# Optimization experiments

Hardware: AMD Instinct MI355X
Metric: run time of the kernel (lower is better)

## Reference

```python
import jax, jax.numpy as jnp
import numpy as np

RNN = 512
ENC = 512
HID = 512
ATT_SIZE = 196
B = 1024


def setup_inputs() -> dict:
    key = jax.random.key(0)
    ks = jax.random.split(key, 20)
    s = 0.02
    d = {
        "h": jax.random.normal(ks[0], (B, RNN), jnp.float32),
        "sentinel": jax.random.normal(ks[1], (B, RNN), jnp.float32),
        "att_feats": jax.random.normal(ks[2], (B, ATT_SIZE, RNN), jnp.float32),
        "W_ctx2att": jax.random.normal(ks[3], (RNN, HID), jnp.float32) * s,
        "b_ctx2att": jnp.zeros((HID,), jnp.float32),
        "W_sl": jax.random.normal(ks[4], (RNN, ENC), jnp.float32) * s,
        "b_sl": jnp.zeros((ENC,), jnp.float32),
        "W_se": jax.random.normal(ks[5], (ENC, HID), jnp.float32) * s,
        "b_se": jnp.zeros((HID,), jnp.float32),
        "W_hl": jax.random.normal(ks[6], (RNN, ENC), jnp.float32) * s,
        "b_hl": jnp.zeros((ENC,), jnp.float32),
        "W_he": jax.random.normal(ks[7], (ENC, HID), jnp.float32) * s,
        "b_he": jnp.zeros((HID,), jnp.float32),
        "W_alpha": jax.random.normal(ks[8], (HID, 1), jnp.float32) * s,
        "b_alpha": jnp.zeros((1,), jnp.float32),
        "W_att2h": jax.random.normal(ks[9], (RNN, RNN), jnp.float32) * s,
        "b_att2h": jnp.zeros((RNN,), jnp.float32),
    }
    return d


def reference(h, sentinel, att_feats, W_ctx2att, b_ctx2att, W_sl, b_sl,
              W_se, b_se, W_hl, b_hl, W_he, b_he, W_alpha, b_alpha,
              W_att2h, b_att2h):
    # Eval mode: dropout is identity.
    # Project attention features: [B, 196, HID]
    p_att = jnp.einsum("bsd,dh->bsh", att_feats, W_ctx2att) + b_ctx2att
    # Sentinel branch
    sent_lin = jax.nn.relu(sentinel @ W_sl + b_sl)          # [B, ENC]
    sent_emb = sent_lin @ W_se + b_se                       # [B, HID]
    # Hidden-state branch
    h_lin = jnp.tanh(h @ W_hl + b_hl)                       # [B, ENC]
    h_emb = h_lin @ W_he + b_he                             # [B, HID]
    # Concat sentinel with visual features: [B, 197, *]
    img_all = jnp.concatenate([sent_lin[:, None, :], att_feats], axis=1)
    img_all_embed = jnp.concatenate([sent_emb[:, None, :], p_att], axis=1)
    # Additive attention scores over 197 positions
    hA = jnp.tanh(img_all_embed + h_emb[:, None, :])        # [B, 197, HID]
    scores = (jnp.einsum("bsh,ho->bso", hA, W_alpha) + b_alpha)[..., 0]  # [B, 197]
    alpha = jax.nn.softmax(scores, axis=-1)
    # Weighted context
    cHat = jnp.einsum("bs,bsd->bd", alpha, img_all)          # [B, RNN]
    atten_out = cHat + h_lin
    out = jnp.tanh(atten_out @ W_att2h + b_att2h)            # [B, RNN]
    return out
```

## Files before the change

kernel.cpp:

```cpp
#include <hip/hip_runtime.h>
#include <hip/hip_bf16.h>

#define KDIM 512
#define NDIM 512
#define ATT  196
#define NB   1024

typedef __attribute__((ext_vector_type(8))) short bf16x8;
typedef __attribute__((ext_vector_type(8))) unsigned short ushort8;
typedef __attribute__((ext_vector_type(4))) float f32x4;

typedef const __attribute__((address_space(1))) unsigned int gas_uint;
typedef __attribute__((address_space(3))) unsigned int las_uint;

__device__ __forceinline__ void gload16(const void* g, void* l) {
    __builtin_amdgcn_global_load_lds((gas_uint*)g, (las_uint*)l, 16, 0, 0);
}

__device__ __forceinline__ float fast_tanh(float x) {
    x = fminf(15.f, fmaxf(-15.f, x));
    float t = __expf(2.f * x);
    return (t - 1.f) / (t + 1.f);
}

__device__ __forceinline__ unsigned short f2bf(float x) {
    union { float f; unsigned u; } v; v.f = x;
    unsigned r = v.u + 0x7FFF + ((v.u >> 16) & 1);
    return (unsigned short)(r >> 16);
}

__device__ __forceinline__ unsigned pk2(float a, float b) {
    __hip_bfloat162 h = __float22bfloat162_rn(float2{a, b});
    union { __hip_bfloat162 h2; unsigned u; } c; c.h2 = h;
    return c.u;
}

__global__ __launch_bounds__(256) void prep_weights(
        const float* __restrict__ W0, const float* __restrict__ W1,
        const float* __restrict__ W2, const float* __restrict__ W3,
        const float* __restrict__ W4, const float* __restrict__ W5,
        unsigned short* __restrict__ Wt) {
    int w = blockIdx.x >> 6;
    int t = blockIdx.x & 63;
    int k0 = (t >> 3) << 6, n0 = (t & 7) << 6;
    const float* W = (w == 0) ? W0 : (w == 1) ? W1 : (w == 2) ? W2 :
                     (w == 3) ? W3 : (w == 4) ? W4 : W5;
    __shared__ float tile[64][65];
    int tid = threadIdx.x;
    int nc = tid & 15, kr = tid >> 4;
#pragma unroll
    for (int i = 0; i < 4; ++i) {
        int k = kr + i * 16;
        float4 v = *(const float4*)&W[(size_t)(k0 + k) * NDIM + n0 + nc * 4];
        tile[k][nc * 4 + 0] = v.x; tile[k][nc * 4 + 1] = v.y;
        tile[k][nc * 4 + 2] = v.z; tile[k][nc * 4 + 3] = v.w;
    }
    __syncthreads();
    int n = tid >> 2, ks = tid & 3;
    ushort8 v0, v1;
#pragma unroll
    for (int j = 0; j < 8; ++j) v0[j] = f2bf(tile[ks * 16 + j][n]);
#pragma unroll
    for (int j = 0; j < 8; ++j) v1[j] = f2bf(tile[ks * 16 + 8 + j][n]);
    size_t base = ((size_t)w << 18) + (size_t)(n0 + n) * KDIM + k0 + ks * 16;
    *(ushort8*)&Wt[base] = v0;
    *(ushort8*)&Wt[base + 8] = v1;
}

__global__ __launch_bounds__(256) void gemm64(
        const float* __restrict__ A0, const unsigned short* __restrict__ W0,
        const float* __restrict__ bia0, float* __restrict__ O0, int act0,
        const float* __restrict__ A1, const unsigned short* __restrict__ W1,
        const float* __restrict__ bia1, float* __restrict__ O1, int act1) {
    const int op = blockIdx.y;
    const float* A = op ? A1 : A0;
    const unsigned short* Bt = op ? W1 : W0;
    const float* bias = op ? bia1 : bia0;
    float* out = op ? O1 : O0;
    const int act = op ? act1 : act0;

    __shared__ unsigned short A_lds[2][64 * 32];
    __shared__ unsigned short B_lds[2][128 * 32];

    const int tid = threadIdx.x;
    const int gm0 = (blockIdx.x >> 2) * 64, gn0 = (blockIdx.x & 3) * 128;
    const int wid = tid >> 6, lane = tid & 63;
    const int wm = wid >> 1, wn = wid & 1;
    const int lr = lane & 15, lk = lane >> 4;

    const int arow = tid >> 2, akc = tid & 3;
    const float* aptr = A + (size_t)(gm0 + arow) * KDIM + akc * 8;
    const int aoff = arow * 32 + ((akc ^ ((arow >> 1) & 3)) << 3);

    auto stageB = [&](int kt, int buf) {
#pragma unroll
        for (int j = 0; j < 2; ++j) {
            int c = tid + j * 256;
            int col = c >> 2, slot = c & 3;
            const unsigned short* src = Bt + (size_t)(gn0 + col) * KDIM +
                                        ((slot ^ ((col >> 1) & 3)) << 3) + kt * 32;
            gload16(src, &B_lds[buf][c * 8]);
        }
    };

    f32x4 acc[2][4] = {};

    {
        float4 x0 = *(const float4*)aptr;
        float4 x1 = *(const float4*)(aptr + 4);
        stageB(0, 0);
        uint4 p;
        p.x = pk2(x0.x, x0.y); p.y = pk2(x0.z, x0.w);
        p.z = pk2(x1.x, x1.y); p.w = pk2(x1.z, x1.w);
        *(uint4*)&A_lds[0][aoff] = p;
    }
    __syncthreads();

    const int swk = ((lk ^ ((lr >> 1) & 3)) << 3);
    for (int kt = 0; kt < 16; ++kt) {
        const int buf = kt & 1;
        float4 x0, x1;
        if (kt < 15) {
            const float* ap = aptr + (kt + 1) * 32;
            x0 = *(const float4*)ap;
            x1 = *(const float4*)(ap + 4);
            stageB(kt + 1, buf ^ 1);
        }
        bf16x8 af[2], bfr[4];
#pragma unroll
        for (int m = 0; m < 2; ++m)
            af[m] = *(const bf16x8*)&A_lds[buf][(wm * 32 + m * 16 + lr) * 32 + swk];
#pragma unroll
        for (int n = 0; n < 4; ++n)
            bfr[n] = *(const bf16x8*)&B_lds[buf][(wn * 64 + n * 16 + lr) * 32 + swk];
#pragma unroll
        for (int m = 0; m < 2; ++m)
#pragma unroll
            for (int n = 0; n < 4; ++n)
                acc[m][n] = __builtin_amdgcn_mfma_f32_16x16x32_bf16(af[m], bfr[n], acc[m][n], 0, 0, 0);
        if (kt < 15) {
            uint4 p;
            p.x = pk2(x0.x, x0.y); p.y = pk2(x0.z, x0.w);
            p.z = pk2(x1.x, x1.y); p.w = pk2(x1.z, x1.w);
            *(uint4*)&A_lds[buf ^ 1][aoff] = p;
        }
        __syncthreads();
    }

#pragma unroll
    for (int m = 0; m < 2; ++m)
#pragma unroll
        for (int n = 0; n < 4; ++n) {
            int col = gn0 + wn * 64 + n * 16 + lr;
            float bsv = bias[col];
#pragma unroll
            for (int r = 0; r < 4; ++r) {
                int row = gm0 + wm * 32 + m * 16 + lk * 4 + r;
                float v = acc[m][n][r] + bsv;
                if (act == 0) v = fmaxf(v, 0.f);
                else if (act == 1) v = fast_tanh(v);
                out[(size_t)row * NDIM + col] = v;
            }
        }
}

__launch_bounds__(256, 3)
__global__ void gemm_score(const float* __restrict__ A,
                           const unsigned short* __restrict__ Bt,
                           const float* __restrict__ b_ctx,
                           const float* __restrict__ h_emb,
                           const float* __restrict__ Walpha,
                           float* __restrict__ score) {
    __shared__ unsigned short A_lds[2][128 * 32];
    __shared__ unsigned short B_lds[2][128 * 32];
    __shared__ float ch_s[2][128];
    __shared__ float wa_s[128];
    __shared__ float s_red[2][128];

    const int tid  = threadIdx.x;
    const int bidx = blockIdx.x;
    const int xcd  = bidx & 7, u = bidx >> 3;
    const int mblk = xcd * 196 + (u >> 2), nblk = u & 3;
    const int gm0  = mblk * 128, gn0 = nblk * 128;

    const int wid = tid >> 6, lane = tid & 63;
    const int wm  = wid >> 1, wn = wid & 1;
    const int lr  = lane & 15, lk = lane >> 4;

    const int b0 = gm0 / ATT;
    {
        int j = tid >> 7, cloc = tid & 127;
        int bb = b0 + j; if (bb > NB - 1) bb = NB - 1;
        ch_s[j][cloc] = b_ctx[gn0 + cloc] + h_emb[(size_t)bb * NDIM + gn0 + cloc];
        if (tid < 128) wa_s[tid] = Walpha[gn0 + tid];
    }

    const int arow = tid >> 1, ahalf = tid & 1;
    const float* aptr = A + (size_t)(gm0 + arow) * KDIM + ahalf * 16;
    const int skc0  = (ahalf * 2) ^ ((arow >> 1) & 3);
    const int aoff0 = arow * 32 + skc0 * 8;
    const int aoff1 = arow * 32 + (skc0 ^ 1) * 8;

    auto stageB = [&](int kt, int buf) {
#pragma unroll
        for (int j = 0; j < 2; ++j) {
            int c = tid + j * 256;
            int col = c >> 2, slot = c & 3;
            const unsigned short* src = Bt + (size_t)(gn0 + col) * KDIM +
                                        ((slot ^ ((col >> 1) & 3)) << 3) + kt * 32;
            gload16(src, &B_lds[buf][c * 8]);
        }
    };

    f32x4 acc[4][4] = {};

    {
        float4 x0 = *(const float4*)(aptr);
        float4 x1 = *(const float4*)(aptr + 4);
        float4 x2 = *(const float4*)(aptr + 8);
        float4 x3 = *(const float4*)(aptr + 12);
        stageB(0, 0);
        uint4 p0, p1;
        p0.x = pk2(x0.x, x0.y); p0.y = pk2(x0.z, x0.w);
        p0.z = pk2(x1.x, x1.y); p0.w = pk2(x1.z, x1.w);
        p1.x = pk2(x2.x, x2.y); p1.y = pk2(x2.z, x2.w);
        p1.z = pk2(x3.x, x3.y); p1.w = pk2(x3.z, x3.w);
        *(uint4*)&A_lds[0][aoff0] = p0;
        *(uint4*)&A_lds[0][aoff1] = p1;
    }
    __syncthreads();

    const int swk = ((lk ^ ((lr >> 1) & 3)) << 3);
    for (int kt = 0; kt < 16; ++kt) {
        const int buf = kt & 1;
        float4 x0, x1, x2, x3;
        if (kt < 15) {
            const float* ap = aptr + (kt + 1) * 32;
            x0 = *(const float4*)(ap);
            x1 = *(const float4*)(ap + 4);
            x2 = *(const float4*)(ap + 8);
            x3 = *(const float4*)(ap + 12);
            stageB(kt + 1, buf ^ 1);
        }
        bf16x8 af[4], bfr[4];
#pragma unroll
        for (int m = 0; m < 4; ++m)
            af[m] = *(const bf16x8*)&A_lds[buf][(wm * 64 + m * 16 + lr) * 32 + swk];
#pragma unroll
        for (int n = 0; n < 4; ++n)
            bfr[n] = *(const bf16x8*)&B_lds[buf][(wn * 64 + n * 16 + lr) * 32 + swk];
#pragma unroll
        for (int m = 0; m < 4; ++m)
#pragma unroll
            for (int n = 0; n < 4; ++n)
                acc[m][n] = __builtin_amdgcn_mfma_f32_16x16x32_bf16(af[m], bfr[n], acc[m][n], 0, 0, 0);
        if (kt < 15) {
            uint4 p0, p1;
            p0.x = pk2(x0.x, x0.y); p0.y = pk2(x0.z, x0.w);
            p0.z = pk2(x1.x, x1.y); p0.w = pk2(x1.z, x1.w);
            p1.x = pk2(x2.x, x2.y); p1.y = pk2(x2.z, x2.w);
            p1.z = pk2(x3.x, x3.y); p1.w = pk2(x3.z, x3.w);
            *(uint4*)&A_lds[buf ^ 1][aoff0] = p0;
            *(uint4*)&A_lds[buf ^ 1][aoff1] = p1;
        }
        __syncthreads();
    }

    const int bsplit = (b0 + 1) * ATT;
#pragma unroll
    for (int m = 0; m < 4; ++m) {
#pragma unroll
        for (int r = 0; r < 4; ++r) {
            int rloc = wm * 64 + m * 16 + lk * 4 + r;
            int rg = gm0 + rloc;
            int sel = (rg >= bsplit) ? 1 : 0;
            float sum = 0.f;
#pragma unroll
            for (int n = 0; n < 4; ++n) {
                int cloc = wn * 64 + n * 16 + lr;
                sum += fast_tanh(acc[m][n][r] + ch_s[sel][cloc]) * wa_s[cloc];
            }
            sum += __shfl_xor(sum, 1);
            sum += __shfl_xor(sum, 2);
            sum += __shfl_xor(sum, 4);
            sum += __shfl_xor(sum, 8);
            if (lr == 0) s_red[wn][rloc] = sum;
        }
    }
    __syncthreads();
    if (tid < 128) {
        float tot = s_red[0][tid] + s_red[1][tid];
        int rg = gm0 + tid;
        int sel = (rg >= bsplit) ? 1 : 0;
        int bb = b0 + sel;
        atomicAdd(&score[(size_t)bb * 197 + (rg - bb * ATT) + 1], tot);
    }
}

__global__ __launch_bounds__(256) void softmax_chat(
        const float* __restrict__ score, const float* __restrict__ sent_emb,
        const float* __restrict__ h_emb, const float* __restrict__ Walpha,
        const float* __restrict__ sent_lin, const float* __restrict__ h_lin,
        const float* __restrict__ att, float* __restrict__ atten_out) {
    int b = blockIdx.x, tid = threadIdx.x;
    __shared__ float al[200];
    __shared__ float r4[4];

    float2 se = ((const float2*)(sent_emb + (size_t)b * NDIM))[tid];
    float2 he = ((const float2*)(h_emb + (size_t)b * NDIM))[tid];
    float2 wa = ((const float2*)Walpha)[tid];
    float val = fast_tanh(se.x + he.x) * wa.x + fast_tanh(se.y + he.y) * wa.y;
#pragma unroll
    for (int o = 32; o; o >>= 1) val += __shfl_xor(val, o);
    if ((tid & 63) == 0) r4[tid >> 6] = val;
    __syncthreads();
    float ssent = r4[0] + r4[1] + r4[2] + r4[3];
    __syncthreads();

    float v = -1e30f;
    if (tid < 197) v = (tid == 0) ? ssent : score[(size_t)b * 197 + tid];
    float m = v;
#pragma unroll
    for (int o = 32; o; o >>= 1) m = fmaxf(m, __shfl_xor(m, o));
    if ((tid & 63) == 0) r4[tid >> 6] = m;
    __syncthreads();
    m = fmaxf(fmaxf(r4[0], r4[1]), fmaxf(r4[2], r4[3]));
    __syncthreads();
    float e = (tid < 197) ? __expf(v - m) : 0.f;
    float s = e;
#pragma unroll
    for (int o = 32; o; o >>= 1) s += __shfl_xor(s, o);
    if ((tid & 63) == 0) r4[tid >> 6] = s;
    __syncthreads();
    s = r4[0] + r4[1] + r4[2] + r4[3];
    if (tid < 197) al[tid] = e / s;
    __syncthreads();

    const float2* af = (const float2*)(att + (size_t)b * ATT * KDIM);
    float2 a0 = ((const float2*)(sent_lin + (size_t)b * KDIM))[tid];
    float w0 = al[0];
    float2 accv; accv.x = w0 * a0.x; accv.y = w0 * a0.y;
#pragma unroll 14
    for (int ss = 0; ss < ATT; ++ss) {
        float w = al[ss + 1];
        float2 x = af[(size_t)ss * 256 + tid];
        accv.x += w * x.x; accv.y += w * x.y;
    }
    float2 hl = ((const float2*)(h_lin + (size_t)b * KDIM))[tid];
    accv.x += hl.x; accv.y += hl.y;
    ((float2*)(atten_out + (size_t)b * KDIM))[tid] = accv;
}

extern "C" void kernel_launch(void* const* d_in, const int* in_sizes, int n_in,
                              void* d_out, int out_size, void* d_ws, size_t ws_size,
                              hipStream_t stream) {
    const float* h     = (const float*)d_in[0];
    const float* sent  = (const float*)d_in[1];
    const float* att   = (const float*)d_in[2];
    const float* W_ctx = (const float*)d_in[3];
    const float* b_ctx = (const float*)d_in[4];
    const float* W_sl  = (const float*)d_in[5];
    const float* b_sl  = (const float*)d_in[6];
    const float* W_se  = (const float*)d_in[7];
    const float* b_se  = (const float*)d_in[8];
    const float* W_hl  = (const float*)d_in[9];
    const float* b_hl  = (const float*)d_in[10];
    const float* W_he  = (const float*)d_in[11];
    const float* b_he  = (const float*)d_in[12];
    const float* W_al  = (const float*)d_in[13];
    const float* W_a2h = (const float*)d_in[15];
    const float* b_a2h = (const float*)d_in[16];
    float* out = (float*)d_out;

    char* ws = (char*)d_ws;
    unsigned short* Wt = (unsigned short*)ws;
    float* sent_lin = (float*)(ws + 6u * 512 * 1024);
    float* h_lin    = sent_lin + (size_t)NB * 512;
    float* h_emb    = h_lin    + (size_t)NB * 512;
    float* sent_emb = h_emb    + (size_t)NB * 512;
    float* scorebuf = sent_emb + (size_t)NB * 512;
    float* atten    = scorebuf + (size_t)NB * 197;

    const size_t WSZ = 512 * 512;
    prep_weights<<<384, 256, 0, stream>>>(W_sl, W_hl, W_he, W_ctx, W_a2h, W_se, Wt);
    hipMemsetAsync(scorebuf, 0, (size_t)NB * 197 * sizeof(float), stream);

    gemm64<<<dim3(64, 2), 256, 0, stream>>>(
        sent, Wt + 0 * WSZ, b_sl, sent_lin, 0,
        h,    Wt + 1 * WSZ, b_hl, h_lin,    1);
    gemm64<<<dim3(64, 2), 256, 0, stream>>>(
        h_lin,    Wt + 2 * WSZ, b_he, h_emb,    2,
        sent_lin, Wt + 5 * WSZ, b_se, sent_emb, 2);

    gemm_score<<<6272, 256, 0, stream>>>(att, Wt + 3 * WSZ, b_ctx, h_emb, W_al, scorebuf);

    softmax_chat<<<NB, 256, 0, stream>>>(scorebuf, sent_emb, h_emb, W_al,
                                         sent_lin, h_lin, att, atten);

    gemm64<<<dim3(64, 1), 256, 0, stream>>>(
        atten, Wt + 4 * WSZ, b_a2h, out, 1,
        atten, Wt + 4 * WSZ, b_a2h, out, 1);
}
```

Baseline: 390.6 us.

## Triple-buffer score GEMM LDS with two-stage prefetch and explicit waitcnt barriers

```diff
diff --git a/kernel.cpp b/kernel.cpp
--- a/kernel.cpp
+++ b/kernel.cpp
@@ -171,8 +171,8 @@
                            const float* __restrict__ h_emb,
                            const float* __restrict__ Walpha,
                            float* __restrict__ score) {
-    __shared__ unsigned short A_lds[2][128 * 32];
-    __shared__ unsigned short B_lds[2][128 * 32];
+    __shared__ unsigned short A_lds[3][128 * 32];
+    __shared__ unsigned short B_lds[3][128 * 32];
     __shared__ float ch_s[2][128];
     __shared__ float wa_s[128];
     __shared__ float s_red[2][128];
@@ -187,86 +187,105 @@
     const int wm  = wid >> 1, wn = wid & 1;
     const int lr  = lane & 15, lk = lane >> 4;
 
-    const int b0 = gm0 / ATT;
-    {
-        int j = tid >> 7, cloc = tid & 127;
-        int bb = b0 + j; if (bb > NB - 1) bb = NB - 1;
-        ch_s[j][cloc] = b_ctx[gn0 + cloc] + h_emb[(size_t)bb * NDIM + gn0 + cloc];
-        if (tid < 128) wa_s[tid] = Walpha[gn0 + tid];
-    }
-
     const int arow = tid >> 1, ahalf = tid & 1;
     const float* aptr = A + (size_t)(gm0 + arow) * KDIM + ahalf * 16;
     const int skc0  = (ahalf * 2) ^ ((arow >> 1) & 3);
     const int aoff0 = arow * 32 + skc0 * 8;
     const int aoff1 = arow * 32 + (skc0 ^ 1) * 8;
 
-    auto stageB = [&](int kt, int buf) {
-#pragma unroll
-        for (int j = 0; j < 2; ++j) {
-            int c = tid + j * 256;
-            int col = c >> 2, slot = c & 3;
-            const unsigned short* src = Bt + (size_t)(gn0 + col) * KDIM +
-                                        ((slot ^ ((col >> 1) & 3)) << 3) + kt * 32;
-            gload16(src, &B_lds[buf][c * 8]);
-        }
+    const int c1 = tid + 256;
+    const int bcol0 = tid >> 2, bk0 = (tid & 3) ^ ((bcol0 >> 1) & 3);
+    const int bcol1 = c1 >> 2,  bk1 = (c1 & 3) ^ ((bcol1 >> 1) & 3);
+    const unsigned short* bsrc0 = Bt + (size_t)(gn0 + bcol0) * KDIM + bk0 * 8;
+    const unsigned short* bsrc1 = Bt + (size_t)(gn0 + bcol1) * KDIM + bk1 * 8;
+
+    auto issueB = [&](int kt, int buf) {
+        gload16(bsrc0 + kt * 32, &B_lds[buf][tid * 8]);
+        gload16(bsrc1 + kt * 32, &B_lds[buf][c1 * 8]);
     };
+    auto loadA = [&](int kt, float4* x) {
+        const float* ap = aptr + kt * 32;
+        x[0] = *(const float4*)(ap);
+        x[1] = *(const float4*)(ap + 4);
+        x[2] = *(const float4*)(ap + 8);
+        x[3] = *(const float4*)(ap + 12);
+    };
+    auto writeA = [&](float4* x, int buf) {
+        uint4 p0, p1;
+        p0.x = pk2(x[0].x, x[0].y); p0.y = pk2(x[0].z, x[0].w);
+        p0.z = pk2(x[1].x, x[1].y); p0.w = pk2(x[1].z, x[1].w);
+        p1.x = pk2(x[2].x, x[2].y); p1.y = pk2(x[2].z, x[2].w);
+        p1.z = pk2(x[3].x, x[3].y); p1.w = pk2(x[3].z, x[3].w);
+        *(uint4*)&A_lds[buf][aoff0] = p0;
+        *(uint4*)&A_lds[buf][aoff1] = p1;
+    };
 
     f32x4 acc[4][4] = {};
-
-    {
-        float4 x0 = *(const float4*)(aptr);
-        float4 x1 = *(const float4*)(aptr + 4);
-        float4 x2 = *(const float4*)(aptr + 8);
-        float4 x3 = *(const float4*)(aptr + 12);
-        stageB(0, 0);
-        uint4 p0, p1;
-        p0.x = pk2(x0.x, x0.y); p0.y = pk2(x0.z, x0.w);
-        p0.z = pk2(x1.x, x1.y); p0.w = pk2(x1.z, x1.w);
-        p1.x = pk2(x2.x, x2.y); p1.y = pk2(x2.z, x2.w);
-        p1.z = pk2(x3.x, x3.y); p1.w = pk2(x3.z, x3.w);
-        *(uint4*)&A_lds[0][aoff0] = p0;
-        *(uint4*)&A_lds[0][aoff1] = p1;
-    }
-    __syncthreads();
-
+    float4 xa[4], xb[4];
     const int swk = ((lk ^ ((lr >> 1) & 3)) << 3);
-    for (int kt = 0; kt < 16; ++kt) {
-        const int buf = kt & 1;
-        float4 x0, x1, x2, x3;
-        if (kt < 15) {
-            const float* ap = aptr + (kt + 1) * 32;
-            x0 = *(const float4*)(ap);
-            x1 = *(const float4*)(ap + 4);
-            x2 = *(const float4*)(ap + 8);
-            x3 = *(const float4*)(ap + 12);
-            stageB(kt + 1, buf ^ 1);
-        }
+
+    loadA(0, xa);
+    issueB(0, 0);
+    writeA(xa, 0);
+    loadA(1, xa);
+    issueB(1, 1);
+    asm volatile("s_waitcnt vmcnt(6) lgkmcnt(0)" ::: "memory");
+    __builtin_amdgcn_sched_barrier(0);
+    __builtin_amdgcn_s_barrier();
+    __builtin_amdgcn_sched_barrier(0);
+
+    auto body = [&](int t, int bT, int bT1, int bT2, float4* xc, float4* xn) {
+        if (t + 2 < 16) {
+            loadA(t + 2, xn);
+            issueB(t + 2, bT2);
+        }
+        __builtin_amdgcn_sched_barrier(0);
         bf16x8 af[4], bfr[4];
 #pragma unroll
         for (int m = 0; m < 4; ++m)
-            af[m] = *(const bf16x8*)&A_lds[buf][(wm * 64 + m * 16 + lr) * 32 + swk];
+            af[m] = *(const bf16x8*)&A_lds[bT][(wm * 64 + m * 16 + lr) * 32 + swk];
 #pragma unroll
         for (int n = 0; n < 4; ++n)
-            bfr[n] = *(const bf16x8*)&B_lds[buf][(wn * 64 + n * 16 + lr) * 32 + swk];
+            bfr[n] = *(const bf16x8*)&B_lds[bT][(wn * 64 + n * 16 + lr) * 32 + swk];
 #pragma unroll
         for (int m = 0; m < 4; ++m)
 #pragma unroll
             for (int n = 0; n < 4; ++n)
                 acc[m][n] = __builtin_amdgcn_mfma_f32_16x16x32_bf16(af[m], bfr[n], acc[m][n], 0, 0, 0);
-        if (kt < 15) {
-            uint4 p0, p1;
-            p0.x = pk2(x0.x, x0.y); p0.y = pk2(x0.z, x0.w);
-            p0.z = pk2(x1.x, x1.y); p0.w = pk2(x1.z, x1.w);
-            p1.x = pk2(x2.x, x2.y); p1.y = pk2(x2.z, x2.w);
-            p1.z = pk2(x3.x, x3.y); p1.w = pk2(x3.z, x3.w);
-            *(uint4*)&A_lds[buf ^ 1][aoff0] = p0;
-            *(uint4*)&A_lds[buf ^ 1][aoff1] = p1;
-        }
-        __syncthreads();
-    }
-
-    const int bsplit = (b0 + 1) * ATT;
+        if (t + 1 < 16) writeA(xc, bT1);
+        if (t < 15) {
+            if (t + 2 < 16) {
+                asm volatile("s_waitcnt vmcnt(6) lgkmcnt(0)" ::: "memory");
+            } else {
+                asm volatile("s_waitcnt vmcnt(0) lgkmcnt(0)" ::: "memory");
+            }
+            __builtin_amdgcn_sched_barrier(0);
+            __builtin_amdgcn_s_barrier();
+            __builtin_amdgcn_sched_barrier(0);
+        }
+    };
+
+    int q0 = 0;
+#pragma unroll 1
+    for (int tt = 0; tt < 16; tt += 2) {
+        int q1 = (q0 == 2) ? 0 : q0 + 1;
+        int q2 = (q1 == 2) ? 0 : q1 + 1;
+        int q3 = (q2 == 2) ? 0 : q2 + 1;
+        body(tt,     q0, q1, q2, xa, xb);
+        body(tt + 1, q1, q2, q3, xb, xa);
+        q0 = q2;
+    }
+
+    const int bb0 = gm0 / ATT;
+    {
+        int j = tid >> 7, cloc = tid & 127;
+        int bb = bb0 + j; if (bb > NB - 1) bb = NB - 1;
+        ch_s[j][cloc] = b_ctx[gn0 + cloc] + h_emb[(size_t)bb * NDIM + gn0 + cloc];
+        if (tid < 128) wa_s[tid] = Walpha[gn0 + tid];
+    }
+    __syncthreads();
+
+    const int bsplit = (bb0 + 1) * ATT;
 #pragma unroll
     for (int m = 0; m < 4; ++m) {
 #pragma unroll
@@ -292,7 +311,7 @@
         float tot = s_red[0][tid] + s_red[1][tid];
         int rg = gm0 + tid;
         int sel = (rg >= bsplit) ? 1 : 0;
-        int bb = b0 + sel;
+        int bb = bb0 + sel;
         atomicAdd(&score[(size_t)bb * 197 + (rg - bb * ATT) + 1], tot);
     }
 }
```

Measured after the change: 391.5 us. About the same (+0.2%).

## Load A fragments directly from global into registers, bypassing LDS staging

Applied to the files above, without the earlier changes.

```diff
diff --git a/kernel.cpp b/kernel.cpp
--- a/kernel.cpp
+++ b/kernel.cpp
@@ -171,7 +171,6 @@
                            const float* __restrict__ h_emb,
                            const float* __restrict__ Walpha,
                            float* __restrict__ score) {
-    __shared__ unsigned short A_lds[2][128 * 32];
     __shared__ unsigned short B_lds[2][128 * 32];
     __shared__ float ch_s[2][128];
     __shared__ float wa_s[128];
@@ -187,86 +186,87 @@
     const int wm  = wid >> 1, wn = wid & 1;
     const int lr  = lane & 15, lk = lane >> 4;
 
-    const int b0 = gm0 / ATT;
+    const int bb0 = gm0 / ATT;
     {
         int j = tid >> 7, cloc = tid & 127;
-        int bb = b0 + j; if (bb > NB - 1) bb = NB - 1;
+        int bb = bb0 + j; if (bb > NB - 1) bb = NB - 1;
         ch_s[j][cloc] = b_ctx[gn0 + cloc] + h_emb[(size_t)bb * NDIM + gn0 + cloc];
         if (tid < 128) wa_s[tid] = Walpha[gn0 + tid];
     }
 
-    const int arow = tid >> 1, ahalf = tid & 1;
-    const float* aptr = A + (size_t)(gm0 + arow) * KDIM + ahalf * 16;
-    const int skc0  = (ahalf * 2) ^ ((arow >> 1) & 3);
-    const int aoff0 = arow * 32 + skc0 * 8;
-    const int aoff1 = arow * 32 + (skc0 ^ 1) * 8;
+    const float* ap0 = A + (size_t)(gm0 + wm * 64 + 0 * 16 + lr) * KDIM + lk * 8;
+    const float* ap1 = A + (size_t)(gm0 + wm * 64 + 1 * 16 + lr) * KDIM + lk * 8;
+    const float* ap2 = A + (size_t)(gm0 + wm * 64 + 2 * 16 + lr) * KDIM + lk * 8;
+    const float* ap3 = A + (size_t)(gm0 + wm * 64 + 3 * 16 + lr) * KDIM + lk * 8;
+
+    const int c1 = tid + 256;
+    const int bcol0 = tid >> 2, bk0 = (tid & 3) ^ ((bcol0 >> 1) & 3);
+    const int bcol1 = c1 >> 2,  bk1 = (c1 & 3) ^ ((bcol1 >> 1) & 3);
+    const unsigned short* bsrc0 = Bt + (size_t)(gn0 + bcol0) * KDIM + bk0 * 8;
+    const unsigned short* bsrc1 = Bt + (size_t)(gn0 + bcol1) * KDIM + bk1 * 8;
 
     auto stageB = [&](int kt, int buf) {
-#pragma unroll
-        for (int j = 0; j < 2; ++j) {
-            int c = tid + j * 256;
-            int col = c >> 2, slot = c & 3;
-            const unsigned short* src = Bt + (size_t)(gn0 + col) * KDIM +
-                                        ((slot ^ ((col >> 1) & 3)) << 3) + kt * 32;
-            gload16(src, &B_lds[buf][c * 8]);
-        }
+        gload16(bsrc0 + kt * 32, &B_lds[buf][tid * 8]);
+        gload16(bsrc1 + kt * 32, &B_lds[buf][c1 * 8]);
     };
 
     f32x4 acc[4][4] = {};
-
-    {
-        float4 x0 = *(const float4*)(aptr);
-        float4 x1 = *(const float4*)(aptr + 4);
-        float4 x2 = *(const float4*)(aptr + 8);
-        float4 x3 = *(const float4*)(aptr + 12);
-        stageB(0, 0);
-        uint4 p0, p1;
-        p0.x = pk2(x0.x, x0.y); p0.y = pk2(x0.z, x0.w);
-        p0.z = pk2(x1.x, x1.y); p0.w = pk2(x1.z, x1.w);
-        p1.x = pk2(x2.x, x2.y); p1.y = pk2(x2.z, x2.w);
-        p1.z = pk2(x3.x, x3.y); p1.w = pk2(x3.z, x3.w);
-        *(uint4*)&A_lds[0][aoff0] = p0;
-        *(uint4*)&A_lds[0][aoff1] = p1;
-    }
-    __syncthreads();
-
     const int swk = ((lk ^ ((lr >> 1) & 3)) << 3);
-    for (int kt = 0; kt < 16; ++kt) {
-        const int buf = kt & 1;
-        float4 x0, x1, x2, x3;
-        if (kt < 15) {
-            const float* ap = aptr + (kt + 1) * 32;
-            x0 = *(const float4*)(ap);
-            x1 = *(const float4*)(ap + 4);
-            x2 = *(const float4*)(ap + 8);
-            x3 = *(const float4*)(ap + 12);
-            stageB(kt + 1, buf ^ 1);
-        }
-        bf16x8 af[4], bfr[4];
-#pragma unroll
-        for (int m = 0; m < 4; ++m)
-            af[m] = *(const bf16x8*)&A_lds[buf][(wm * 64 + m * 16 + lr) * 32 + swk];
-#pragma unroll
-        for (int n = 0; n < 4; ++n)
-            bfr[n] = *(const bf16x8*)&B_lds[buf][(wn * 64 + n * 16 + lr) * 32 + swk];
-#pragma unroll
-        for (int m = 0; m < 4; ++m)
-#pragma unroll
-            for (int n = 0; n < 4; ++n)
-                acc[m][n] = __builtin_amdgcn_mfma_f32_16x16x32_bf16(af[m], bfr[n], acc[m][n], 0, 0, 0);
-        if (kt < 15) {
-            uint4 p0, p1;
-            p0.x = pk2(x0.x, x0.y); p0.y = pk2(x0.z, x0.w);
-            p0.z = pk2(x1.x, x1.y); p0.w = pk2(x1.z, x1.w);
-            p1.x = pk2(x2.x, x2.y); p1.y = pk2(x2.z, x2.w);
-            p1.z = pk2(x3.x, x3.y); p1.w = pk2(x3.z, x3.w);
-            *(uint4*)&A_lds[buf ^ 1][aoff0] = p0;
-            *(uint4*)&A_lds[buf ^ 1][aoff1] = p1;
-        }
+
+#define LOAD_A(kt, s) \
+    s##0a = *(const float4*)(ap0 + (kt) * 32); s##0b = *(const float4*)(ap0 + (kt) * 32 + 4); \
+    s##1a = *(const float4*)(ap1 + (kt) * 32); s##1b = *(const float4*)(ap1 + (kt) * 32 + 4); \
+    s##2a = *(const float4*)(ap2 + (kt) * 32); s##2b = *(const float4*)(ap2 + (kt) * 32 + 4); \
+    s##3a = *(const float4*)(ap3 + (kt) * 32); s##3b = *(const float4*)(ap3 + (kt) * 32 + 4);
+
+#define CVT1(ya, yb, dst) { \
+    uint4 p; \
+    p.x = pk2(ya.x, ya.y); p.y = pk2(ya.z, ya.w); \
+    p.z = pk2(yb.x, yb.y); p.w = pk2(yb.z, yb.w); \
+    union { uint4 u; bf16x8 v; } cc; cc.u = p; dst = cc.v; }
+
+#define COMPUTE(s, buf) { \
+    bf16x8 bfr[4]; \
+    _Pragma("unroll") \
+    for (int n = 0; n < 4; ++n) \
+        bfr[n] = *(const bf16x8*)&B_lds[buf][(wn * 64 + n * 16 + lr) * 32 + swk]; \
+    bf16x8 a0, a1, a2, a3; \
+    CVT1(s##0a, s##0b, a0); CVT1(s##1a, s##1b, a1); \
+    CVT1(s##2a, s##2b, a2); CVT1(s##3a, s##3b, a3); \
+    _Pragma("unroll") \
+    for (int n = 0; n < 4; ++n) acc[0][n] = __builtin_amdgcn_mfma_f32_16x16x32_bf16(a0, bfr[n], acc[0][n], 0, 0, 0); \
+    _Pragma("unroll") \
+    for (int n = 0; n < 4; ++n) acc[1][n] = __builtin_amdgcn_mfma_f32_16x16x32_bf16(a1, bfr[n], acc[1][n], 0, 0, 0); \
+    _Pragma("unroll") \
+    for (int n = 0; n < 4; ++n) acc[2][n] = __builtin_amdgcn_mfma_f32_16x16x32_bf16(a2, bfr[n], acc[2][n], 0, 0, 0); \
+    _Pragma("unroll") \
+    for (int n = 0; n < 4; ++n) acc[3][n] = __builtin_amdgcn_mfma_f32_16x16x32_bf16(a3, bfr[n], acc[3][n], 0, 0, 0); }
+
+    float4 fx0a, fx0b, fx1a, fx1b, fx2a, fx2b, fx3a, fx3b;
+    float4 fy0a, fy0b, fy1a, fy1b, fy2a, fy2b, fy3a, fy3b;
+
+    LOAD_A(0, fx);
+    stageB(0, 0);
+    __syncthreads();
+
+#pragma unroll 1
+    for (int kt = 0; kt < 16; kt += 2) {
+        LOAD_A(kt + 1, fy);
+        stageB(kt + 1, 1);
+        COMPUTE(fx, 0);
         __syncthreads();
-    }
-
-    const int bsplit = (b0 + 1) * ATT;
+        if (kt + 2 < 16) {
+            LOAD_A(kt + 2, fx);
+            stageB(kt + 2, 0);
+        }
+        COMPUTE(fy, 1);
+        __syncthreads();
+    }
+#undef LOAD_A
+#undef CVT1
+#undef COMPUTE
+
+    const int bsplit = (bb0 + 1) * ATT;
 #pragma unroll
     for (int m = 0; m < 4; ++m) {
 #pragma unroll
@@ -292,7 +292,7 @@
         float tot = s_red[0][tid] + s_red[1][tid];
         int rg = gm0 + tid;
         int sel = (rg >= bsplit) ? 1 : 0;
-        int bb = b0 + sel;
+        int bb = bb0 + sel;
         atomicAdd(&score[(size_t)bb * 197 + (rg - bb * ATT) + 1], tot);
     }
 }
```

Measured after the change: 535.7 us. 37.1% more time.

## Stage fp32 A tiles via direct global-to-LDS loads, convert to bf16 at fragment read

Applied to the files above, without the earlier changes.

```diff
diff --git a/kernel.cpp b/kernel.cpp
--- a/kernel.cpp
+++ b/kernel.cpp
@@ -171,7 +171,7 @@
                            const float* __restrict__ h_emb,
                            const float* __restrict__ Walpha,
                            float* __restrict__ score) {
-    __shared__ unsigned short A_lds[2][128 * 32];
+    __shared__ float A_f[2][128 * 32];
     __shared__ unsigned short B_lds[2][128 * 32];
     __shared__ float ch_s[2][128];
     __shared__ float wa_s[128];
@@ -187,86 +187,80 @@
     const int wm  = wid >> 1, wn = wid & 1;
     const int lr  = lane & 15, lk = lane >> 4;
 
-    const int b0 = gm0 / ATT;
+    const int bb0 = gm0 / ATT;
     {
         int j = tid >> 7, cloc = tid & 127;
-        int bb = b0 + j; if (bb > NB - 1) bb = NB - 1;
+        int bb = bb0 + j; if (bb > NB - 1) bb = NB - 1;
         ch_s[j][cloc] = b_ctx[gn0 + cloc] + h_emb[(size_t)bb * NDIM + gn0 + cloc];
         if (tid < 128) wa_s[tid] = Walpha[gn0 + tid];
     }
 
-    const int arow = tid >> 1, ahalf = tid & 1;
-    const float* aptr = A + (size_t)(gm0 + arow) * KDIM + ahalf * 16;
-    const int skc0  = (ahalf * 2) ^ ((arow >> 1) & 3);
-    const int aoff0 = arow * 32 + skc0 * 8;
-    const int aoff1 = arow * 32 + (skc0 ^ 1) * 8;
-
+    const float* asrc[4];
+#pragma unroll
+    for (int i = 0; i < 4; ++i) {
+        int c = tid + i * 256;
+        int row = c >> 3, g = c & 7;
+        int srcg = g ^ (row & 7);
+        asrc[i] = A + (size_t)(gm0 + row) * KDIM + srcg * 4;
+    }
+    auto stageA = [&](int kt, int buf) {
+#pragma unroll
+        for (int i = 0; i < 4; ++i)
+            gload16(asrc[i] + kt * 32, &A_f[buf][(tid + i * 256) * 4]);
+    };
+
+    const int c1 = tid + 256;
+    const int bcol0 = tid >> 2, bk0 = (tid & 3) ^ ((bcol0 >> 1) & 3);
+    const int bcol1 = c1 >> 2,  bk1 = (c1 & 3) ^ ((bcol1 >> 1) & 3);
+    const unsigned short* bsrc0 = Bt + (size_t)(gn0 + bcol0) * KDIM + bk0 * 8;
+    const unsigned short* bsrc1 = Bt + (size_t)(gn0 + bcol1) * KDIM + bk1 * 8;
     auto stageB = [&](int kt, int buf) {
-#pragma unroll
-        for (int j = 0; j < 2; ++j) {
-            int c = tid + j * 256;
-            int col = c >> 2, slot = c & 3;
-            const unsigned short* src = Bt + (size_t)(gn0 + col) * KDIM +
-                                        ((slot ^ ((col >> 1) & 3)) << 3) + kt * 32;
-            gload16(src, &B_lds[buf][c * 8]);
-        }
+        gload16(bsrc0 + kt * 32, &B_lds[buf][tid * 8]);
+        gload16(bsrc1 + kt * 32, &B_lds[buf][c1 * 8]);
     };
 
     f32x4 acc[4][4] = {};
-
-    {
-        float4 x0 = *(const float4*)(aptr);
-        float4 x1 = *(const float4*)(aptr + 4);
-        float4 x2 = *(const float4*)(aptr + 8);
-        float4 x3 = *(const float4*)(aptr + 12);
-        stageB(0, 0);
-        uint4 p0, p1;
-        p0.x = pk2(x0.x, x0.y); p0.y = pk2(x0.z, x0.w);
-        p0.z = pk2(x1.x, x1.y); p0.w = pk2(x1.z, x1.w);
-        p1.x = pk2(x2.x, x2.y); p1.y = pk2(x2.z, x2.w);
-        p1.z = pk2(x3.x, x3.y); p1.w = pk2(x3.z, x3.w);
-        *(uint4*)&A_lds[0][aoff0] = p0;
-        *(uint4*)&A_lds[0][aoff1] = p1;
-    }
-    __syncthreads();
-
     const int swk = ((lk ^ ((lr >> 1) & 3)) << 3);
+
+    const int arw = ((wm * 64 + lr) & 7);
+    const int as0 = (lk * 2) ^ arw;
+    const int as1 = (lk * 2 + 1) ^ arw;
+
+    stageA(0, 0);
+    stageB(0, 0);
+    __syncthreads();
+
+#pragma unroll 1
     for (int kt = 0; kt < 16; ++kt) {
         const int buf = kt & 1;
-        float4 x0, x1, x2, x3;
         if (kt < 15) {
-            const float* ap = aptr + (kt + 1) * 32;
-            x0 = *(const float4*)(ap);
-            x1 = *(const float4*)(ap + 4);
-            x2 = *(const float4*)(ap + 8);
-            x3 = *(const float4*)(ap + 12);
+            stageA(kt + 1, buf ^ 1);
             stageB(kt + 1, buf ^ 1);
         }
         bf16x8 af[4], bfr[4];
-#pragma unroll
-        for (int m = 0; m < 4; ++m)
-            af[m] = *(const bf16x8*)&A_lds[buf][(wm * 64 + m * 16 + lr) * 32 + swk];
 #pragma unroll
         for (int n = 0; n < 4; ++n)
             bfr[n] = *(const bf16x8*)&B_lds[buf][(wn * 64 + n * 16 + lr) * 32 + swk];
 #pragma unroll
+        for (int m = 0; m < 4; ++m) {
+            const int rbase = (wm * 64 + m * 16 + lr) * 32;
+            float4 fa = *(const float4*)&A_f[buf][rbase + as0 * 4];
+            float4 fb = *(const float4*)&A_f[buf][rbase + as1 * 4];
+            uint4 p;
+            p.x = pk2(fa.x, fa.y); p.y = pk2(fa.z, fa.w);
+            p.z = pk2(fb.x, fb.y); p.w = pk2(fb.z, fb.w);
+            union { uint4 u; bf16x8 v; } cc; cc.u = p;
+            af[m] = cc.v;
+        }
+#pragma unroll
         for (int m = 0; m < 4; ++m)
 #pragma unroll
             for (int n = 0; n < 4; ++n)
                 acc[m][n] = __builtin_amdgcn_mfma_f32_16x16x32_bf16(af[m], bfr[n], acc[m][n], 0, 0, 0);
-        if (kt < 15) {
-            uint4 p0, p1;
-            p0.x = pk2(x0.x, x0.y); p0.y = pk2(x0.z, x0.w);
-            p0.z = pk2(x1.x, x1.y); p0.w = pk2(x1.z, x1.w);
-            p1.x = pk2(x2.x, x2.y); p1.y = pk2(x2.z, x2.w);
-            p1.z = pk2(x3.x, x3.y); p1.w = pk2(x3.z, x3.w);
-            *(uint4*)&A_lds[buf ^ 1][aoff0] = p0;
-            *(uint4*)&A_lds[buf ^ 1][aoff1] = p1;
-        }
         __syncthreads();
     }
 
-    const int bsplit = (b0 + 1) * ATT;
+    const int bsplit = (bb0 + 1) * ATT;
 #pragma unroll
     for (int m = 0; m < 4; ++m) {
 #pragma unroll
@@ -292,7 +286,7 @@
         float tot = s_red[0][tid] + s_red[1][tid];
         int rg = gm0 + tid;
         int sel = (rg >= bsplit) ? 1 : 0;
-        int bb = b0 + sel;
+        int bb = bb0 + sel;
         atomicAdd(&score[(size_t)bb * 197 + (rg - bb * ATT) + 1], tot);
     }
 }
```

Result: faster. 375.0 us (-4.0%).
